# Optimization experiments

Hardware: AMD Instinct MI355X
Metric: run time of the kernel (lower is better)

The kernel has to match this reference:

```python
import jax, jax.numpy as jnp
import numpy as np
import math

EMBED_DIM = 512
NUM_HEADS = 8
HEAD_DIM = EMBED_DIM // NUM_HEADS


def setup_inputs() -> dict:
    key = jax.random.key(0)
    ks = jax.random.split(key, 11)
    s = 1.0 / math.sqrt(EMBED_DIM)
    x = jax.random.normal(ks[0], (8, EMBED_DIM, 32, 32), dtype=jnp.float32)
    Wq = jax.random.uniform(ks[1], (EMBED_DIM, EMBED_DIM), jnp.float32, -s, s)
    bq = jax.random.uniform(ks[2], (EMBED_DIM,), jnp.float32, -s, s)
    Wk = jax.random.uniform(ks[3], (EMBED_DIM, EMBED_DIM), jnp.float32, -s, s)
    bk = jax.random.uniform(ks[4], (EMBED_DIM,), jnp.float32, -s, s)
    Wv = jax.random.uniform(ks[5], (EMBED_DIM, EMBED_DIM), jnp.float32, -s, s)
    bv = jax.random.uniform(ks[6], (EMBED_DIM,), jnp.float32, -s, s)
    Wo = jax.random.uniform(ks[7], (EMBED_DIM, EMBED_DIM), jnp.float32, -s, s)
    bo = jax.random.uniform(ks[8], (EMBED_DIM,), jnp.float32, -s, s)
    gamma = jnp.ones((EMBED_DIM,), jnp.float32)
    beta = jnp.zeros((EMBED_DIM,), jnp.float32)
    return {"x": x, "Wq": Wq, "bq": bq, "Wk": Wk, "bk": bk, "Wv": Wv,
            "bv": bv, "Wo": Wo, "bo": bo, "gamma": gamma, "beta": beta}


def layer_norm(x, gamma, beta, eps=1e-5):
    mu = jnp.mean(x, axis=-1, keepdims=True)
    var = jnp.mean(jnp.square(x - mu), axis=-1, keepdims=True)
    return (x - mu) * jax.lax.rsqrt(var + eps) * gamma + beta


def reference(x, Wq, bq, Wk, bk, Wv, bv, Wo, bo, gamma, beta):
    B, C, H, W = x.shape
    S = H * W
    # [B, S, C]
    x_flat = x.reshape(B, C, S).transpose(0, 2, 1)
    residual = x_flat
    xn = layer_norm(x_flat, gamma, beta)
    # torch Linear: y = x @ W^T + b
    q = (xn @ Wq.T + bq).reshape(B, S, NUM_HEADS, HEAD_DIM)
    k = (xn @ Wk.T + bk).reshape(B, S, NUM_HEADS, HEAD_DIM)
    v = (xn @ Wv.T + bv).reshape(B, S, NUM_HEADS, HEAD_DIM)
    scale = 1.0 / math.sqrt(HEAD_DIM)
    scores = jnp.einsum('bqhd,bkhd->bhqk', q, k) * scale
    attn = jax.nn.softmax(scores, axis=-1)  # dropout is identity in eval
    out = jnp.einsum('bhqk,bkhd->bqhd', attn, v).reshape(B, S, C)
    out = out @ Wo.T + bo + residual
    return out.transpose(0, 2, 1).reshape(B, C, H, W)
```

## Files before the change

### kernel.cpp

```cpp
#include <hip/hip_runtime.h>
#include <hip/hip_bf16.h>

typedef __bf16 bf16_t;
typedef __bf16 bf16x8 __attribute__((ext_vector_type(8)));
typedef float floatx4 __attribute__((ext_vector_type(4)));

#define EMBED 512
#define S_LEN 1024
#define NH 8
#define HD 64
#define LDK 1056
#define LDV 1088

#define MFMA16(a, b, c) __builtin_amdgcn_mfma_f32_16x16x32_bf16(a, b, c, 0, 0, 0)

static __device__ __forceinline__ bf16_t f2bf(float f) {
    unsigned int x = __builtin_bit_cast(unsigned int, f);
    unsigned int lsb = (x >> 16) & 1u;
    x += 0x7fffu + lsb;
    unsigned short u = (unsigned short)(x >> 16);
    return __builtin_bit_cast(bf16_t, u);
}
static __device__ __forceinline__ float bf2f(bf16_t v) {
    unsigned short u = __builtin_bit_cast(unsigned short, v);
    unsigned int x = ((unsigned int)u) << 16;
    return __builtin_bit_cast(float, x);
}
static __device__ __forceinline__ unsigned int pack2(float lo, float hi) {
    return (__builtin_bit_cast(unsigned int, lo) >> 16) |
           (__builtin_bit_cast(unsigned int, hi) & 0xFFFF0000u);
}
static __device__ __forceinline__ unsigned int pack2r(float lo, float hi) {
    unsigned short a = __builtin_bit_cast(unsigned short, f2bf(lo));
    unsigned short b = __builtin_bit_cast(unsigned short, f2bf(hi));
    return (unsigned int)a | ((unsigned int)b << 16);
}
static __device__ __forceinline__ void gload16(const bf16_t* g, bf16_t* l) {
    __builtin_amdgcn_global_load_lds(
        (const __attribute__((address_space(1))) unsigned int*)g,
        (__attribute__((address_space(3))) unsigned int*)l, 16, 0, 0);
}

__global__ __launch_bounds__(256) void cvt4_kernel(const float* __restrict__ s0,
                                                   const float* __restrict__ s1,
                                                   const float* __restrict__ s2,
                                                   const float* __restrict__ s3,
                                                   bf16_t* __restrict__ d0,
                                                   bf16_t* __restrict__ d1,
                                                   bf16_t* __restrict__ d2,
                                                   bf16_t* __restrict__ d3) {
    const float* s; bf16_t* d;
    switch (blockIdx.y) {
        case 0:  s = s0; d = d0; break;
        case 1:  s = s1; d = d1; break;
        case 2:  s = s2; d = d2; break;
        default: s = s3; d = d3; break;
    }
    int i = (blockIdx.x * 256 + threadIdx.x) * 8;
#pragma unroll
    for (int j = 0; j < 8; ++j) d[i + j] = f2bf(s[i + j]);
}

__global__ __launch_bounds__(256) void ln_fused_kernel(const float* __restrict__ x,
                                                       const float* __restrict__ gamma,
                                                       const float* __restrict__ beta,
                                                       bf16_t* __restrict__ xn) {
    __shared__ float T[32][521];
    __shared__ float Pm[32][33], Pq[32][33];
    __shared__ float Mu[32], Rs[32];
    int bid = blockIdx.x;
    int b = bid >> 5, s0 = (bid & 31) * 32;
    int t = threadIdx.x;
    int lc = t >> 3;
    int si = (t & 7) * 4;
    const float* xp = x + ((size_t)b * EMBED + lc) * S_LEN + s0 + si;
    float sm[4] = {}, sq[4] = {};
#pragma unroll
    for (int p = 0; p < 16; ++p) {
        int c = lc + p * 32;
        float4 v = *(const float4*)(xp + (size_t)p * 32 * S_LEN);
        int cs = c ^ ((c >> 3) & 0x38);
        T[si + 0][cs] = v.x; T[si + 1][cs] = v.y;
        T[si + 2][cs] = v.z; T[si + 3][cs] = v.w;
        sm[0] += v.x; sq[0] += v.x * v.x;
        sm[1] += v.y; sq[1] += v.y * v.y;
        sm[2] += v.z; sq[2] += v.z * v.z;
        sm[3] += v.w; sq[3] += v.w * v.w;
    }
#pragma unroll
    for (int k = 0; k < 4; ++k) { Pm[si + k][lc] = sm[k]; Pq[si + k][lc] = sq[k]; }
    __syncthreads();
    if (t < 32) {
        float m = 0.f, q = 0.f;
#pragma unroll
        for (int j = 0; j < 32; ++j) { m += Pm[t][j]; q += Pq[t][j]; }
        float mu = m * (1.0f / EMBED);
        float var = q * (1.0f / EMBED) - mu * mu;
        Mu[t] = mu; Rs[t] = rsqrtf(var + 1e-5f);
    }
    __syncthreads();
    int cidx = t & 31;
    int rw = t >> 5;
#pragma unroll
    for (int rg = 0; rg < 4; ++rg) {
        int srl = rg * 8 + rw;
        float mu = Mu[srl], rs = Rs[srl];
        int cb = cidx * 16;
        bf16_t* dst = xn + ((size_t)b * S_LEN + s0 + srl) * EMBED + cb;
#pragma unroll
        for (int h = 0; h < 2; ++h) {
            int c0h = cb + h * 8;
            float4 g0 = *(const float4*)(gamma + c0h);
            float4 g1 = *(const float4*)(gamma + c0h + 4);
            float4 be0 = *(const float4*)(beta + c0h);
            float4 be1 = *(const float4*)(beta + c0h + 4);
            float gv[8] = {g0.x, g0.y, g0.z, g0.w, g1.x, g1.y, g1.z, g1.w};
            float bv[8] = {be0.x, be0.y, be0.z, be0.w, be1.x, be1.y, be1.z, be1.w};
            bf16x8 o;
#pragma unroll
            for (int j = 0; j < 8; ++j) {
                int c = c0h + j;
                int cs = c ^ ((c >> 3) & 0x38);
                o[j] = f2bf((T[srl][cs] - mu) * rs * gv[j] + bv[j]);
            }
            *(bf16x8*)(dst + h * 8) = o;
        }
    }
}

__global__ __launch_bounds__(256) void gemm_kernel(const bf16_t* __restrict__ X,
                                                   const bf16_t* __restrict__ W,
                                                   const float* __restrict__ b0,
                                                   const float* __restrict__ b1,
                                                   const float* __restrict__ b2,
                                                   bf16_t* __restrict__ Y,
                                                   bf16_t* __restrict__ vtb) {
    __shared__ __align__(16) bf16_t Sh[2][128 * 72];
    bf16_t* Wlin = &Sh[0][0];
    int t = threadIdx.x;
    int col0 = blockIdx.y * 128, row0 = blockIdx.x * 128;
    int lane = t & 63, w = t >> 6, g = lane >> 4, n16 = lane & 15;
    int swzk = (((lane & 7) ^ (lane >> 3)) & 7) * 8;
    const bf16_t* wg = W + (size_t)(col0 + w * 32 + (lane >> 3)) * EMBED + swzk;
    bf16_t* ldwave = Wlin + (w * 4) * 512;
    {
#pragma unroll
        for (int j = 0; j < 4; ++j)
            gload16(wg + (size_t)j * 8 * EMBED, ldwave + j * 512);
    }
    int rw0 = row0 + w * 32;
    const bf16_t* xr0 = X + (size_t)(rw0 + n16) * EMBED + g * 8;
    const bf16_t* xr1 = xr0 + (size_t)16 * EMBED;
    bf16x8 a00 = *(const bf16x8*)(xr0);
    bf16x8 a01 = *(const bf16x8*)(xr0 + 32);
    bf16x8 a10 = *(const bf16x8*)(xr1);
    bf16x8 a11 = *(const bf16x8*)(xr1 + 32);
    __syncthreads();
    floatx4 acc[2][8] = {};
    int cs0 = ((g ^ (n16 & 7))) * 8;
#pragma unroll
    for (int kc = 0; kc < 8; ++kc) {
        bf16x8 na00, na01, na10, na11;
        if (kc < 7) {
            int ko = (kc + 1) * 64;
            bf16_t* ld = Wlin + ((kc + 1) & 1) * 8192 + (w * 4) * 512;
#pragma unroll
            for (int j = 0; j < 4; ++j)
                gload16(wg + (size_t)j * 8 * EMBED + ko, ld + j * 512);
            na00 = *(const bf16x8*)(xr0 + ko);
            na01 = *(const bf16x8*)(xr0 + ko + 32);
            na10 = *(const bf16x8*)(xr1 + ko);
            na11 = *(const bf16x8*)(xr1 + ko + 32);
        }
        const bf16_t* wb = Wlin + (kc & 1) * 8192;
#pragma unroll
        for (int kk = 0; kk < 2; ++kk) {
            bf16x8 s0 = (kk == 0) ? a00 : a01;
            bf16x8 s1 = (kk == 0) ? a10 : a11;
            int csk = cs0 ^ (kk * 32);
#pragma unroll
            for (int nt = 0; nt < 8; ++nt) {
                bf16x8 bfr = *(const bf16x8*)(&wb[(nt * 16 + n16) * 64 + csk]);
                acc[0][nt] = MFMA16(s0, bfr, acc[0][nt]);
                acc[1][nt] = MFMA16(s1, bfr, acc[1][nt]);
            }
        }
        if (kc < 7) {
            a00 = na00; a01 = na01; a10 = na10; a11 = na11;
        }
        __syncthreads();
    }
    if (col0 < 1024) {
        const float* bp = (col0 < 512) ? b0 : b1;
#pragma unroll
        for (int ar = 0; ar < 2; ++ar)
#pragma unroll
            for (int nt = 0; nt < 8; ++nt) {
                int col = col0 + nt * 16 + n16;
                float bv = bp[col & 511];
#pragma unroll
                for (int r = 0; r < 4; ++r) {
                    int row = rw0 + ar * 16 + g * 4 + r;
                    Y[(size_t)row * LDK + col] = f2bf(acc[ar][nt][r] + bv);
                }
            }
    } else {
        bf16_t* Tl = Wlin;
#pragma unroll
        for (int ar = 0; ar < 2; ++ar)
#pragma unroll
            for (int nt = 0; nt < 8; ++nt) {
                int chl = nt * 16 + n16;
                float bv = b2[(col0 & 511) + chl];
                uint2 pr;
                pr.x = pack2r(acc[ar][nt][0] + bv, acc[ar][nt][1] + bv);
                pr.y = pack2r(acc[ar][nt][2] + bv, acc[ar][nt][3] + bv);
                *(uint2*)(&Tl[chl * 136 + w * 32 + ar * 16 + g * 4]) = pr;
            }
        __syncthreads();
        int ch = t >> 1, seg = (t & 1) * 64;
        int bb = row0 >> 10, s0 = row0 & 1023;
        bf16_t* dst = vtb + ((size_t)(bb * EMBED + (col0 - 1024) + ch)) * LDV + s0 + seg;
        const bf16_t* srcl = &Tl[ch * 136 + seg];
#pragma unroll
        for (int i = 0; i < 8; ++i)
            *(bf16x8*)(dst + i * 8) = *(const bf16x8*)(srcl + i * 8);
    }
}

__global__ __launch_bounds__(256) void wsgemm_out_kernel(const bf16_t* __restrict__ Wb,
                                                         const bf16_t* __restrict__ act,
                                                         const float* __restrict__ bias,
                                                         const float* __restrict__ xres,
                                                         float* __restrict__ out) {
    __shared__ __align__(16) bf16_t Al[2][64 * 72];
    int b = blockIdx.z, n0 = blockIdx.x * 64, m0 = blockIdx.y * 128;
    int t = threadIdx.x;
    int srow = t >> 2, sseg = (t & 3) * 16;
    const bf16_t* asrc = act + ((size_t)b * S_LEN + n0 + srow) * EMBED + sseg;
    {
        bf16x8 r0 = *(const bf16x8*)(asrc);
        bf16x8 r1 = *(const bf16x8*)(asrc + 8);
        bf16_t* d = &Al[0][srow * 72 + sseg];
        *(bf16x8*)d = r0; *(bf16x8*)(d + 8) = r1;
    }
    int lane = t & 63, w = t >> 6, g = lane >> 4, n16 = lane & 15;
    int mw = m0 + w * 32;
    const bf16_t* wr0 = Wb + (size_t)(mw + n16) * EMBED + g * 8;
    const bf16_t* wr1 = wr0 + (size_t)16 * EMBED;
    bf16x8 a00 = *(const bf16x8*)(wr0);
    bf16x8 a01 = *(const bf16x8*)(wr0 + 32);
    bf16x8 a10 = *(const bf16x8*)(wr1);
    bf16x8 a11 = *(const bf16x8*)(wr1 + 32);
    __syncthreads();
    floatx4 acc[2][4] = {};
#pragma unroll
    for (int kc = 0; kc < 8; ++kc) {
        bf16x8 p0, p1, na00, na01, na10, na11;
        if (kc < 7) {
            int ko = (kc + 1) * 64;
            p0 = *(const bf16x8*)(asrc + ko);
            p1 = *(const bf16x8*)(asrc + ko + 8);
            na00 = *(const bf16x8*)(wr0 + ko);
            na01 = *(const bf16x8*)(wr0 + ko + 32);
            na10 = *(const bf16x8*)(wr1 + ko);
            na11 = *(const bf16x8*)(wr1 + ko + 32);
        }
        const bf16_t* al = &Al[kc & 1][0];
#pragma unroll
        for (int kk = 0; kk < 2; ++kk) {
            bf16x8 s0 = (kk == 0) ? a00 : a01;
            bf16x8 s1 = (kk == 0) ? a10 : a11;
#pragma unroll
            for (int nt = 0; nt < 4; ++nt) {
                bf16x8 bfr = *(const bf16x8*)(&al[(nt * 16 + n16) * 72 + kk * 32 + g * 8]);
                acc[0][nt] = MFMA16(s0, bfr, acc[0][nt]);
                acc[1][nt] = MFMA16(s1, bfr, acc[1][nt]);
            }
        }
        if (kc < 7) {
            bf16_t* d = &Al[(kc + 1) & 1][srow * 72 + sseg];
            *(bf16x8*)d = p0; *(bf16x8*)(d + 8) = p1;
            a00 = na00; a01 = na01; a10 = na10; a11 = na11;
        }
        __syncthreads();
    }
#pragma unroll
    for (int ar = 0; ar < 2; ++ar)
#pragma unroll
        for (int r = 0; r < 4; ++r) {
            int row = mw + ar * 16 + g * 4 + r;
            float bv = bias[row];
#pragma unroll
            for (int nt = 0; nt < 4; ++nt) {
                int col = n0 + nt * 16 + n16;
                size_t oi = ((size_t)b * EMBED + row) * S_LEN + col;
                out[oi] = acc[ar][nt][r] + bv + xres[oi];
            }
        }
}

__global__ __launch_bounds__(256) void attn_kernel(const bf16_t* __restrict__ qk,
                                                   const bf16_t* __restrict__ vt,
                                                   bf16_t* __restrict__ o) {
    __shared__ __align__(16) bf16_t Kt[2][64 * 72];
    __shared__ __align__(16) bf16_t Vl2[2][64 * 72];
    __shared__ __align__(16) unsigned int Pl[4][16 * 68];
    int bid = blockIdx.x;
    int bh = bid & 63, qt = bid >> 6;
    int b = bh >> 3, h = bh & 7;
    int t = threadIdx.x, w = t >> 6, lane = t & 63, g = lane >> 4, n16 = lane & 15;
    size_t baseQK = (size_t)b * S_LEN * LDK;
    size_t baseV  = ((size_t)b * EMBED + h * HD) * LDV;
    int qA = qt * 128 + w * 32 + n16;

    const float QSC = 0.18033688f;
    const bf16_t* qpA = qk + baseQK + (size_t)qA * LDK + h * HD + g * 8;
    const bf16_t* qpB = qpA + (size_t)16 * LDK;
    bf16x8 qa0 = *(const bf16x8*)(qpA);
    bf16x8 qa1 = *(const bf16x8*)(qpA + 32);
    bf16x8 qb0 = *(const bf16x8*)(qpB);
    bf16x8 qb1 = *(const bf16x8*)(qpB + 32);
#pragma unroll
    for (int j = 0; j < 8; ++j) {
        qa0[j] = f2bf(bf2f(qa0[j]) * QSC);
        qa1[j] = f2bf(bf2f(qa1[j]) * QSC);
        qb0[j] = f2bf(bf2f(qb0[j]) * QSC);
        qb1[j] = f2bf(bf2f(qb1[j]) * QSC);
    }
    const bf16_t* kbase = qk + baseQK + 512 + h * HD;
    const bf16_t* vbase = vt + baseV;

    int srow = t >> 2, scol = (t & 3) * 16;
    const bf16_t* ksrc = kbase + (size_t)srow * LDK + scol;
    const bf16_t* vsrc = vbase + (size_t)srow * LDV + scol;
    {
        bf16x8 k0 = *(const bf16x8*)(ksrc);
        bf16x8 k1 = *(const bf16x8*)(ksrc + 8);
        bf16x8 v0 = *(const bf16x8*)(vsrc);
        bf16x8 v1 = *(const bf16x8*)(vsrc + 8);
        bf16_t* kd = &Kt[0][srow * 72 + scol];
        bf16_t* vd = &Vl2[0][srow * 72 + scol];
        *(bf16x8*)kd = k0; *(bf16x8*)(kd + 8) = k1;
        *(bf16x8*)vd = v0; *(bf16x8*)(vd + 8) = v1;
    }

    float lsA[4] = {}, lsB[4] = {};
    floatx4 oaccA[4] = {}, oaccB[4] = {};
    unsigned int* PLw = &Pl[w][0];
    const float NEG12L2E = -17.3123405f;

    for (int it = 0; it < 16; ++it) {
        int cur = it & 1, nxt = cur ^ 1;
        __syncthreads();
        bf16x8 pk0, pk1, pv0, pv1;
        if (it < 15) {
            const bf16_t* kp = ksrc + (size_t)(it + 1) * 64 * LDK;
            pk0 = *(const bf16x8*)(kp);
            pk1 = *(const bf16x8*)(kp + 8);
            const bf16_t* vp = vsrc + (it + 1) * 64;
            pv0 = *(const bf16x8*)(vp);
            pv1 = *(const bf16x8*)(vp + 8);
        }
        const bf16_t* Kl = &Kt[cur][0];
        const bf16_t* Vl = &Vl2[cur][0];
        floatx4 sA[4], sB[4];
        __builtin_amdgcn_s_setprio(1);
#pragma unroll
        for (int kb = 0; kb < 4; ++kb) {
            bf16x8 k0 = *(const bf16x8*)(&Kl[(kb * 16 + n16) * 72 + g * 8]);
            bf16x8 k1 = *(const bf16x8*)(&Kl[(kb * 16 + n16) * 72 + 32 + g * 8]);
            sA[kb] = floatx4{NEG12L2E, NEG12L2E, NEG12L2E, NEG12L2E};
            sA[kb] = MFMA16(k0, qa0, sA[kb]);
            sA[kb] = MFMA16(k1, qa1, sA[kb]);
            sB[kb] = floatx4{NEG12L2E, NEG12L2E, NEG12L2E, NEG12L2E};
            sB[kb] = MFMA16(k0, qb0, sB[kb]);
            sB[kb] = MFMA16(k1, qb1, sB[kb]);
        }
        __builtin_amdgcn_s_setprio(0);
#pragma unroll
        for (int kb = 0; kb < 4; ++kb)
#pragma unroll
            for (int r = 0; r < 4; ++r) {
                float eA = exp2f(sA[kb][r]);
                sA[kb][r] = eA; lsA[kb] += eA;
                float eB = exp2f(sB[kb][r]);
                sB[kb][r] = eB; lsB[kb] += eB;
            }
#pragma unroll
        for (int kb = 0; kb < 4; ++kb) {
            uint2 prA, prB;
            prA.x = pack2(sA[kb][0], sA[kb][1]);
            prA.y = pack2(sA[kb][2], sA[kb][3]);
            *(uint2*)&PLw[n16 * 68 + kb * 8 + g * 2] = prA;
            prB.x = pack2(sB[kb][0], sB[kb][1]);
            prB.y = pack2(sB[kb][2], sB[kb][3]);
            *(uint2*)&PLw[n16 * 68 + 32 + kb * 8 + g * 2] = prB;
        }
        uint4 uA0 = *(const uint4*)&PLw[n16 * 68 + g * 4];
        uint4 uA1 = *(const uint4*)&PLw[n16 * 68 + 16 + g * 4];
        uint4 uB0 = *(const uint4*)&PLw[n16 * 68 + 32 + g * 4];
        uint4 uB1 = *(const uint4*)&PLw[n16 * 68 + 48 + g * 4];
        bf16x8 pfA0 = __builtin_bit_cast(bf16x8, uA0);
        bf16x8 pfA1 = __builtin_bit_cast(bf16x8, uA1);
        bf16x8 pfB0 = __builtin_bit_cast(bf16x8, uB0);
        bf16x8 pfB1 = __builtin_bit_cast(bf16x8, uB1);
        if (it < 15) {
            bf16_t* kd = &Kt[nxt][srow * 72 + scol];
            bf16_t* vd = &Vl2[nxt][srow * 72 + scol];
            *(bf16x8*)kd = pk0; *(bf16x8*)(kd + 8) = pk1;
            *(bf16x8*)vd = pv0; *(bf16x8*)(vd + 8) = pv1;
        }
        __builtin_amdgcn_s_setprio(1);
#pragma unroll
        for (int dt = 0; dt < 4; ++dt) {
            bf16x8 v0 = *(const bf16x8*)(&Vl[(dt * 16 + n16) * 72 + g * 8]);
            bf16x8 v1 = *(const bf16x8*)(&Vl[(dt * 16 + n16) * 72 + 32 + g * 8]);
            oaccA[dt] = MFMA16(v0, pfA0, oaccA[dt]);
            oaccA[dt] = MFMA16(v1, pfA1, oaccA[dt]);
            oaccB[dt] = MFMA16(v0, pfB0, oaccB[dt]);
            oaccB[dt] = MFMA16(v1, pfB1, oaccB[dt]);
        }
        __builtin_amdgcn_s_setprio(0);
    }
    float lA = (lsA[0] + lsA[1]) + (lsA[2] + lsA[3]);
    lA += __shfl_xor(lA, 16);
    lA += __shfl_xor(lA, 32);
    float lB = (lsB[0] + lsB[1]) + (lsB[2] + lsB[3]);
    lB += __shfl_xor(lB, 16);
    lB += __shfl_xor(lB, 32);
    float rlA = 1.0f / lA, rlB = 1.0f / lB;
    size_t orowA = ((size_t)b * S_LEN + qA) * EMBED + h * HD;
    size_t orowB = orowA + (size_t)16 * EMBED;
#pragma unroll
    for (int dt = 0; dt < 4; ++dt) {
        uint2 prA, prB;
        prA.x = pack2(oaccA[dt][0] * rlA, oaccA[dt][1] * rlA);
        prA.y = pack2(oaccA[dt][2] * rlA, oaccA[dt][3] * rlA);
        *(uint2*)(o + orowA + dt * 16 + g * 4) = prA;
        prB.x = pack2(oaccB[dt][0] * rlB, oaccB[dt][1] * rlB);
        prB.y = pack2(oaccB[dt][2] * rlB, oaccB[dt][3] * rlB);
        *(uint2*)(o + orowB + dt * 16 + g * 4) = prB;
    }
}

extern "C" void kernel_launch(void* const* d_in, const int* in_sizes, int n_in,
                              void* d_out, int out_size, void* d_ws, size_t ws_size,
                              hipStream_t stream) {
    const float* x     = (const float*)d_in[0];
    const float* Wq    = (const float*)d_in[1];
    const float* bq    = (const float*)d_in[2];
    const float* Wk    = (const float*)d_in[3];
    const float* bk    = (const float*)d_in[4];
    const float* Wv    = (const float*)d_in[5];
    const float* bv    = (const float*)d_in[6];
    const float* Wo    = (const float*)d_in[7];
    const float* bo    = (const float*)d_in[8];
    const float* gamma = (const float*)d_in[9];
    const float* beta  = (const float*)d_in[10];
    float* out = (float*)d_out;

    char* ws = (char*)d_ws;
    bf16_t* xn    = (bf16_t*)ws;
    bf16_t* qkb   = (bf16_t*)(ws + 8388608);
    bf16_t* wqkv  = (bf16_t*)(ws + 25690112);
    bf16_t* wo    = (bf16_t*)(ws + 27262976);
    bf16_t* ab    = xn;

    bf16_t* vtb = (bf16_t*)d_out;

    cvt4_kernel<<<dim3(128, 4), 256, 0, stream>>>(Wq, Wk, Wv, Wo,
                                                  wqkv, wqkv + 262144,
                                                  wqkv + 524288, wo);
    ln_fused_kernel<<<dim3(256), 256, 0, stream>>>(x, gamma, beta, xn);
    gemm_kernel<<<dim3(64, 12), 256, 0, stream>>>(xn, wqkv, bq, bk, bv, qkb, vtb);
    attn_kernel<<<dim3(512), 256, 0, stream>>>(qkb, vtb, ab);
    wsgemm_out_kernel<<<dim3(16, 4, 8), 256, 0, stream>>>(wo, ab, bo, x, out);
}
```

Baseline: 170.0 us.

## Merge weight conversion into layernorm launch, halve LN tile, drop setprio in attention

Weight fp32-to-bf16 conversion and the layernorm/transpose now run in a single launch, with blocks at index 512 and above doing conversion. The layernorm tile shrinks from 32 to 16 sequence positions, which doubles its block count to 512 and gives better occupancy across CUs. The s_setprio hints around the MFMA sections in the attention kernel are removed. Together these aim to cut one launch's overhead and the tail effects of a small grid, at the cost of less per-block reuse and a possible change in wave scheduling inside attention.

```diff
diff --git a/kernel.cpp b/kernel.cpp
--- a/kernel.cpp
+++ b/kernel.cpp
@@ -41,44 +41,46 @@
         (__attribute__((address_space(3))) unsigned int*)l, 16, 0, 0);
 }
 
-__global__ __launch_bounds__(256) void cvt4_kernel(const float* __restrict__ s0,
-                                                   const float* __restrict__ s1,
-                                                   const float* __restrict__ s2,
-                                                   const float* __restrict__ s3,
-                                                   bf16_t* __restrict__ d0,
-                                                   bf16_t* __restrict__ d1,
-                                                   bf16_t* __restrict__ d2,
-                                                   bf16_t* __restrict__ d3) {
-    const float* s; bf16_t* d;
-    switch (blockIdx.y) {
-        case 0:  s = s0; d = d0; break;
-        case 1:  s = s1; d = d1; break;
-        case 2:  s = s2; d = d2; break;
-        default: s = s3; d = d3; break;
-    }
-    int i = (blockIdx.x * 256 + threadIdx.x) * 8;
-#pragma unroll
-    for (int j = 0; j < 8; ++j) d[i + j] = f2bf(s[i + j]);
-}
-
-__global__ __launch_bounds__(256) void ln_fused_kernel(const float* __restrict__ x,
-                                                       const float* __restrict__ gamma,
-                                                       const float* __restrict__ beta,
-                                                       bf16_t* __restrict__ xn) {
-    __shared__ float T[32][521];
-    __shared__ float Pm[32][33], Pq[32][33];
-    __shared__ float Mu[32], Rs[32];
+__global__ __launch_bounds__(256) void ln_cvt_kernel(const float* __restrict__ x,
+                                                     const float* __restrict__ gamma,
+                                                     const float* __restrict__ beta,
+                                                     bf16_t* __restrict__ xn,
+                                                     const float* __restrict__ w0,
+                                                     const float* __restrict__ w1,
+                                                     const float* __restrict__ w2,
+                                                     const float* __restrict__ w3,
+                                                     bf16_t* __restrict__ d0,
+                                                     bf16_t* __restrict__ d1,
+                                                     bf16_t* __restrict__ d2,
+                                                     bf16_t* __restrict__ d3) {
+    __shared__ float T[16][521];
+    __shared__ float Pm[16][65], Pq[16][65];
+    __shared__ float Mu[16], Rs[16];
     int bid = blockIdx.x;
-    int b = bid >> 5, s0 = (bid & 31) * 32;
     int t = threadIdx.x;
-    int lc = t >> 3;
-    int si = (t & 7) * 4;
+    if (bid >= 512) {
+        int cb2 = bid - 512;
+        const float* s; bf16_t* d;
+        switch (cb2 >> 7) {
+            case 0:  s = w0; d = d0; break;
+            case 1:  s = w1; d = d1; break;
+            case 2:  s = w2; d = d2; break;
+            default: s = w3; d = d3; break;
+        }
+        int i = ((cb2 & 127) * 256 + t) * 8;
+#pragma unroll
+        for (int j = 0; j < 8; ++j) d[i + j] = f2bf(s[i + j]);
+        return;
+    }
+    int b = bid >> 6, s0 = (bid & 63) * 16;
+    int lc = t >> 2;
+    int si = (t & 3) * 4;
     const float* xp = x + ((size_t)b * EMBED + lc) * S_LEN + s0 + si;
     float sm[4] = {}, sq[4] = {};
 #pragma unroll
-    for (int p = 0; p < 16; ++p) {
-        int c = lc + p * 32;
-        float4 v = *(const float4*)(xp + (size_t)p * 32 * S_LEN);
+    for (int p = 0; p < 8; ++p) {
+        int c = lc + p * 64;
+        float4 v = *(const float4*)(xp + (size_t)p * 64 * S_LEN);
         int cs = c ^ ((c >> 3) & 0x38);
         T[si + 0][cs] = v.x; T[si + 1][cs] = v.y;
         T[si + 2][cs] = v.z; T[si + 3][cs] = v.w;
@@ -90,10 +92,10 @@
 #pragma unroll
     for (int k = 0; k < 4; ++k) { Pm[si + k][lc] = sm[k]; Pq[si + k][lc] = sq[k]; }
     __syncthreads();
-    if (t < 32) {
+    if (t < 16) {
         float m = 0.f, q = 0.f;
 #pragma unroll
-        for (int j = 0; j < 32; ++j) { m += Pm[t][j]; q += Pq[t][j]; }
+        for (int j = 0; j < 64; ++j) { m += Pm[t][j]; q += Pq[t][j]; }
         float mu = m * (1.0f / EMBED);
         float var = q * (1.0f / EMBED) - mu * mu;
         Mu[t] = mu; Rs[t] = rsqrtf(var + 1e-5f);
@@ -102,7 +104,7 @@
     int cidx = t & 31;
     int rw = t >> 5;
 #pragma unroll
-    for (int rg = 0; rg < 4; ++rg) {
+    for (int rg = 0; rg < 2; ++rg) {
         int srl = rg * 8 + rw;
         float mu = Mu[srl], rs = Rs[srl];
         int cb = cidx * 16;
@@ -365,7 +367,6 @@
         const bf16_t* Kl = &Kt[cur][0];
         const bf16_t* Vl = &Vl2[cur][0];
         floatx4 sA[4], sB[4];
-        __builtin_amdgcn_s_setprio(1);
 #pragma unroll
         for (int kb = 0; kb < 4; ++kb) {
             bf16x8 k0 = *(const bf16x8*)(&Kl[(kb * 16 + n16) * 72 + g * 8]);
@@ -377,7 +378,6 @@
             sB[kb] = MFMA16(k0, qb0, sB[kb]);
             sB[kb] = MFMA16(k1, qb1, sB[kb]);
         }
-        __builtin_amdgcn_s_setprio(0);
 #pragma unroll
         for (int kb = 0; kb < 4; ++kb)
 #pragma unroll
@@ -411,7 +411,6 @@
             *(bf16x8*)kd = pk0; *(bf16x8*)(kd + 8) = pk1;
             *(bf16x8*)vd = pv0; *(bf16x8*)(vd + 8) = pv1;
         }
-        __builtin_amdgcn_s_setprio(1);
 #pragma unroll
         for (int dt = 0; dt < 4; ++dt) {
             bf16x8 v0 = *(const bf16x8*)(&Vl[(dt * 16 + n16) * 72 + g * 8]);
@@ -421,7 +420,6 @@
             oaccB[dt] = MFMA16(v0, pfB0, oaccB[dt]);
             oaccB[dt] = MFMA16(v1, pfB1, oaccB[dt]);
         }
-        __builtin_amdgcn_s_setprio(0);
     }
     float lA = (lsA[0] + lsA[1]) + (lsA[2] + lsA[3]);
     lA += __shfl_xor(lA, 16);
@@ -469,10 +467,10 @@
 
     bf16_t* vtb = (bf16_t*)d_out;
 
-    cvt4_kernel<<<dim3(128, 4), 256, 0, stream>>>(Wq, Wk, Wv, Wo,
+    ln_cvt_kernel<<<dim3(1024), 256, 0, stream>>>(x, gamma, beta, xn,
+                                                  Wq, Wk, Wv, Wo,
                                                   wqkv, wqkv + 262144,
                                                   wqkv + 524288, wo);
-    ln_fused_kernel<<<dim3(256), 256, 0, stream>>>(x, gamma, beta, xn);
     gemm_kernel<<<dim3(64, 12), 256, 0, stream>>>(xn, wqkv, bq, bk, bv, qkb, vtb);
     attn_kernel<<<dim3(512), 256, 0, stream>>>(qkb, vtb, ab);
     wsgemm_out_kernel<<<dim3(16, 4, 8), 256, 0, stream>>>(wo, ab, bo, x, out);
```

Result: no change. 170.0 us (-0.0%).
